# Performance work log

Hardware: AMD Instinct MI355X
Metric: run time of the kernel (lower is better)

Reference implementation:

```python
import jax, jax.numpy as jnp
import numpy as np

B, T, C, H = 16, 2048, 768, 128

def setup_inputs() -> dict:
    key = jax.random.key(0)
    k1, k2, k3, k4 = jax.random.split(key, 4)
    x = jax.random.normal(k1, (B, T, C), dtype=jnp.float32)
    Wq = jax.random.normal(k2, (C, H), dtype=jnp.float32) * (C ** -0.5)
    Wk = jax.random.normal(k3, (C, H), dtype=jnp.float32) * (C ** -0.5)
    Wv = jax.random.normal(k4, (C, H), dtype=jnp.float32) * (C ** -0.5)
    return {"x": x, "Wq": Wq, "Wk": Wk, "Wv": Wv}

def reference(x, Wq, Wk, Wv):
    Bc, Tc, Cc = x.shape
    q = jnp.einsum('btc,ch->bth', x, Wq)
    k = jnp.einsum('btc,ch->bth', x, Wk)
    v = jnp.einsum('btc,ch->bth', x, Wv)
    wei = jnp.einsum('bqh,bkh->bqk', q, k)  # [B,T,T]
    tril = jnp.tril(jnp.ones((Tc, Tc), dtype=jnp.float32))
    # Faithful to original: mask with -inf FIRST, then scale by C**-0.5
    wei = jnp.where(tril == 0, -jnp.inf, wei) * (Cc ** -0.5)
    wei = jax.nn.softmax(wei, axis=-1)
    out = jnp.einsum('bqk,bkh->bqh', wei, v)
    return out
```

## Files before the change

kernel.cpp:

```cpp
#include <hip/hip_runtime.h>
#include <hip/hip_bf16.h>
#include <cstdint>

#define B_ 16
#define T_ 2048
#define C_ 768
#define H_ 128

typedef __bf16 bf16x8 __attribute__((ext_vector_type(8)));
typedef float f32x4 __attribute__((ext_vector_type(4)));
typedef unsigned short u16x8 __attribute__((ext_vector_type(8)));

__device__ __forceinline__ void gld_lds16(const void* g, void* s) {
    __builtin_amdgcn_global_load_lds(
        (__attribute__((address_space(1))) void*)(size_t)g,
        (__attribute__((address_space(3))) void*)s,
        16, 0, 0);
}

__device__ __forceinline__ unsigned short f2bf(float f) {
    __bf16 h = (__bf16)f;
    return __builtin_bit_cast(unsigned short, h);
}

__global__ __launch_bounds__(256) void wconv_kernel(
    const float* __restrict__ Wq, const float* __restrict__ Wk,
    const float* __restrict__ Wv, unsigned short* __restrict__ wT) {
    int idx = blockIdx.x * 256 + threadIdx.x;
    if (idx >= 3 * H_ * C_) return;
    int w = idx / (H_ * C_);
    int r = idx % (H_ * C_);
    int h = r / C_;
    int c = r % C_;
    const float* W = (w == 0) ? Wq : ((w == 1) ? Wk : Wv);
    wT[idx] = f2bf(W[c * H_ + h]);
}

__global__ __launch_bounds__(512, 2) void proj_kernel(
    const float* __restrict__ x, const unsigned short* __restrict__ wT,
    unsigned short* __restrict__ qb, unsigned short* __restrict__ kb,
    unsigned short* __restrict__ vtb) {
    __shared__ unsigned short Asm[2][128 * 64];
    __shared__ unsigned short Bsm[2][192 * 64];

    const int tid = threadIdx.x;
    const int nh = blockIdx.x & 1;
    const int m0 = (blockIdx.x >> 1) * 128;
    const int wid = tid >> 6;
    const int lane = tid & 63;
    const int quad = lane >> 4;
    const int lo16 = lane & 15;
    const int mh = (wid >> 2) * 64;
    const int wnl = (wid & 3) * 48;
    const unsigned short* wTn = wT + (size_t)nh * 192 * C_;

    const int am0 = (tid * 2) >> 4;
    (void)am0;

    f32x4 acc[4][3] = {};
    f32x4 pre[4];

#pragma unroll
    for (int r = 0; r < 2; ++r) {
        int cidx = r * 512 + tid;
        int m = cidx >> 3, lc = cidx & 7;
        const float* src = x + (size_t)(m0 + m) * C_ + lc * 8;
        pre[r * 2] = *(const f32x4*)src;
        pre[r * 2 + 1] = *(const f32x4*)(src + 4);
    }
#pragma unroll
    for (int r = 0; r < 3; ++r) {
        int cidx = r * 512 + tid;
        int n = cidx >> 3, c = (cidx & 7) ^ (n & 7);
        gld_lds16((const char*)wTn + ((size_t)n * C_ + c * 8) * 2,
                  (char*)&Bsm[0][0] + (r * 512 + wid * 64) * 16);
    }
#pragma unroll
    for (int r = 0; r < 2; ++r) {
        int cidx = r * 512 + tid;
        int m = cidx >> 3, lc = cidx & 7;
        u16x8 o;
        o[0] = f2bf(pre[r * 2][0]); o[1] = f2bf(pre[r * 2][1]);
        o[2] = f2bf(pre[r * 2][2]); o[3] = f2bf(pre[r * 2][3]);
        o[4] = f2bf(pre[r * 2 + 1][0]); o[5] = f2bf(pre[r * 2 + 1][1]);
        o[6] = f2bf(pre[r * 2 + 1][2]); o[7] = f2bf(pre[r * 2 + 1][3]);
        *(u16x8*)(&Asm[0][m * 64 + (lc ^ (m & 7)) * 8]) = o;
    }

    for (int kt = 0; kt < 12; ++kt) {
        const int p = kt & 1;
        __syncthreads();
        if (kt + 1 < 12) {
            const int k1 = (kt + 1) * 64;
#pragma unroll
            for (int r = 0; r < 2; ++r) {
                int cidx = r * 512 + tid;
                int m = cidx >> 3, lc = cidx & 7;
                const float* src = x + (size_t)(m0 + m) * C_ + k1 + lc * 8;
                pre[r * 2] = *(const f32x4*)src;
                pre[r * 2 + 1] = *(const f32x4*)(src + 4);
            }
#pragma unroll
            for (int r = 0; r < 3; ++r) {
                int cidx = r * 512 + tid;
                int n = cidx >> 3, c = (cidx & 7) ^ (n & 7);
                gld_lds16((const char*)wTn + ((size_t)n * C_ + k1 + c * 8) * 2,
                          (char*)&Bsm[p ^ 1][0] + (r * 512 + wid * 64) * 16);
            }
        }

#pragma unroll
        for (int kk = 0; kk < 2; ++kk) {
            bf16x8 af[4], bf[3];
#pragma unroll
            for (int mi = 0; mi < 4; ++mi) {
                int m = mh + mi * 16 + lo16;
                int c = (kk * 4 + quad) ^ (m & 7);
                af[mi] = *(const bf16x8*)((const __bf16*)&Asm[p][0] + m * 64 + c * 8);
            }
#pragma unroll
            for (int ni = 0; ni < 3; ++ni) {
                int n = wnl + ni * 16 + lo16;
                int c = (kk * 4 + quad) ^ (n & 7);
                bf[ni] = *(const bf16x8*)((const __bf16*)&Bsm[p][0] + n * 64 + c * 8);
            }
#pragma unroll
            for (int mi = 0; mi < 4; ++mi)
#pragma unroll
                for (int ni = 0; ni < 3; ++ni)
                    acc[mi][ni] = __builtin_amdgcn_mfma_f32_16x16x32_bf16(
                        af[mi], bf[ni], acc[mi][ni], 0, 0, 0);
        }

        if (kt + 1 < 12) {
#pragma unroll
            for (int r = 0; r < 2; ++r) {
                int cidx = r * 512 + tid;
                int m = cidx >> 3, lc = cidx & 7;
                u16x8 o;
                o[0] = f2bf(pre[r * 2][0]); o[1] = f2bf(pre[r * 2][1]);
                o[2] = f2bf(pre[r * 2][2]); o[3] = f2bf(pre[r * 2][3]);
                o[4] = f2bf(pre[r * 2 + 1][0]); o[5] = f2bf(pre[r * 2 + 1][1]);
                o[6] = f2bf(pre[r * 2 + 1][2]); o[7] = f2bf(pre[r * 2 + 1][3]);
                *(u16x8*)(&Asm[p ^ 1][m * 64 + (lc ^ (m & 7)) * 8]) = o;
            }
        }
    }

#pragma unroll
    for (int mi = 0; mi < 4; ++mi) {
        int grow = m0 + mh + mi * 16 + quad * 4;
#pragma unroll
        for (int ni = 0; ni < 3; ++ni) {
            int n = nh * 192 + wnl + ni * 16 + lo16;
            int wmat = n >> 7;
            int col = n & 127;
            if (wmat < 2) {
                unsigned short* o = (wmat == 0) ? qb : kb;
#pragma unroll
                for (int rr = 0; rr < 4; ++rr)
                    o[(size_t)(grow + rr) * H_ + col] = f2bf(acc[mi][ni][rr]);
            } else {
                int b = grow >> 11;
                int t = grow & 2047;
                ushort4 pk;
                pk.x = f2bf(acc[mi][ni][0]); pk.y = f2bf(acc[mi][ni][1]);
                pk.z = f2bf(acc[mi][ni][2]); pk.w = f2bf(acc[mi][ni][3]);
                *(ushort4*)(vtb + ((size_t)b * H_ + col) * T_ + t) = pk;
            }
        }
    }
}

__device__ __forceinline__ void attn_stage(
    const unsigned short* kB, const unsigned short* vB, int kv0, int p,
    unsigned short* Ks, unsigned short* Vs, int tid, int wid) {
#pragma unroll
    for (int rnd = 0; rnd < 4; ++rnd) {
        int cidx = rnd * 256 + tid;
        int m = cidx >> 4;
        int c = (cidx & 15) ^ (m & 15);
        gld_lds16((const char*)kB + ((size_t)(kv0 + m) * H_ + c * 8) * 2,
                  (char*)(Ks + p * 64 * 128) + (rnd * 256 + wid * 64) * 16);
    }
#pragma unroll
    for (int rnd = 0; rnd < 4; ++rnd) {
        int cidx = rnd * 256 + tid;
        int d = cidx >> 3;
        int c = (cidx & 7) ^ (d & 7);
        gld_lds16((const char*)vB + ((size_t)d * T_ + kv0 + c * 8) * 2,
                  (char*)(Vs + p * 128 * 64) + (rnd * 256 + wid * 64) * 16);
    }
}

__device__ __forceinline__ void attn_seg(
    const unsigned short* kB, const unsigned short* vB, const bf16x8 qfrag[4],
    int j0, int j1, int jmask, float& l_part, f32x4 oacc[8],
    unsigned short* Ks, unsigned short* Vs, unsigned short* Pw,
    int tid, int wid, int quad, int lo16) {
    const float cs = 0.05205877694341f;
    __syncthreads();
    attn_stage(kB, vB, j0 * 64, 0, Ks, Vs, tid, wid);
    for (int j = j0; j < j1; ++j) {
        const int p = (j - j0) & 1;
        __syncthreads();
        if (j + 1 < j1) attn_stage(kB, vB, (j + 1) * 64, p ^ 1, Ks, Vs, tid, wid);

        const unsigned short* Kp = Ks + p * 64 * 128;
        const unsigned short* Vp = Vs + p * 128 * 64;

        f32x4 s[4] = {};
#pragma unroll
        for (int ks = 0; ks < 4; ++ks) {
#pragma unroll
            for (int ni = 0; ni < 4; ++ni) {
                int row = ni * 16 + lo16;
                int slot = (ks * 4 + quad) ^ lo16;
                bf16x8 kf = *(const bf16x8*)((const __bf16*)Kp + row * 128 + slot * 8);
                s[ni] = __builtin_amdgcn_mfma_f32_16x16x32_bf16(kf, qfrag[ks], s[ni], 0, 0, 0);
            }
        }

        const bool diag = (j == jmask);
        if (diag) {
#pragma unroll
            for (int ni = 0; ni < 4; ++ni) {
#pragma unroll
                for (int rr = 0; rr < 4; ++rr) {
                    float pv = exp2f(s[ni][rr] * cs);
                    if (ni * 16 + quad * 4 + rr > wid * 16 + lo16) pv = 0.f;
                    l_part += pv;
                    s[ni][rr] = pv;
                }
                ushort4 w4;
                w4.x = f2bf(s[ni][0]); w4.y = f2bf(s[ni][1]);
                w4.z = f2bf(s[ni][2]); w4.w = f2bf(s[ni][3]);
                *(ushort4*)(Pw + lo16 * 72 + ni * 16 + quad * 4) = w4;
            }
        } else {
#pragma unroll
            for (int ni = 0; ni < 4; ++ni) {
#pragma unroll
                for (int rr = 0; rr < 4; ++rr) {
                    float pv = exp2f(s[ni][rr] * cs);
                    l_part += pv;
                    s[ni][rr] = pv;
                }
                ushort4 w4;
                w4.x = f2bf(s[ni][0]); w4.y = f2bf(s[ni][1]);
                w4.z = f2bf(s[ni][2]); w4.w = f2bf(s[ni][3]);
                *(ushort4*)(Pw + lo16 * 72 + ni * 16 + quad * 4) = w4;
            }
        }

#pragma unroll
        for (int ks2 = 0; ks2 < 2; ++ks2) {
            bf16x8 pf = *(const bf16x8*)((const __bf16*)Pw + lo16 * 72 + ks2 * 32 + quad * 8);
#pragma unroll
            for (int nd = 0; nd < 8; ++nd) {
                int dn = nd * 16 + lo16;
                int vc = (ks2 * 4 + quad) ^ (dn & 7);
                bf16x8 vf = *(const bf16x8*)((const __bf16*)Vp + dn * 64 + vc * 8);
                oacc[nd] = __builtin_amdgcn_mfma_f32_16x16x32_bf16(pf, vf, oacc[nd], 0, 0, 0);
            }
        }
    }
}

__device__ __forceinline__ void load_qfrag(const unsigned short* qB, int q0,
                                           int wid, int quad, int lo16, bf16x8 qf[4]) {
    const unsigned short* qrow = qB + (size_t)(q0 + wid * 16 + lo16) * H_ + quad * 8;
#pragma unroll
    for (int ks = 0; ks < 4; ++ks) qf[ks] = *(const bf16x8*)(qrow + ks * 32);
}

__global__ __launch_bounds__(256, 2) void attn_kernel(
    const unsigned short* __restrict__ qb, const unsigned short* __restrict__ kb,
    const unsigned short* __restrict__ vtb, float* __restrict__ out,
    float* __restrict__ pO, float* __restrict__ pL) {
    __shared__ unsigned short Ks[2][64 * 128];
    __shared__ unsigned short Vs[2][128 * 64];
    __shared__ unsigned short Ps[4][16 * 72];

    const int tid = threadIdx.x;
    const int bid = blockIdx.x;
    const int half = bid >> 8;
    const int slot = bid & 255;
    const int r = slot >> 4;
    const int b = slot & 15;

    const unsigned short* qB = qb + (size_t)b * T_ * H_;
    const unsigned short* kB = kb + (size_t)b * T_ * H_;
    const unsigned short* vB = vtb + (size_t)b * H_ * T_;

    const int wid = tid >> 6;
    const int lane = tid & 63;
    const int quad = lane >> 4;
    const int lo16 = lane & 15;
    unsigned short* Pw = &Ps[wid][0];

    const int qtb = 31 - r;
    bf16x8 qf[4];
    float l_part = 0.f;
    f32x4 oacc[8] = {};

    if (half == 0) {
        load_qfrag(qB, r * 64, wid, quad, lo16, qf);
        attn_seg(kB, vB, qf, 0, r + 1, r, l_part, oacc, &Ks[0][0], &Vs[0][0], Pw,
                 tid, wid, quad, lo16);
        l_part += __shfl_xor(l_part, 16);
        l_part += __shfl_xor(l_part, 32);
#pragma unroll
        for (int rr = 0; rr < 4; ++rr) {
            float lv = __shfl(l_part, quad * 4 + rr);
            float inv = 1.0f / lv;
            int qrow = r * 64 + wid * 16 + quad * 4 + rr;
            float* orow = out + ((size_t)b * T_ + qrow) * H_;
#pragma unroll
            for (int nd = 0; nd < 8; ++nd)
                orow[nd * 16 + lo16] = oacc[nd][rr] * inv;
        }
        l_part = 0.f;
#pragma unroll
        for (int nd = 0; nd < 8; ++nd) oacc[nd] = f32x4{0.f, 0.f, 0.f, 0.f};
        load_qfrag(qB, qtb * 64, wid, quad, lo16, qf);
        attn_seg(kB, vB, qf, 0, 16 - r, -1, l_part, oacc, &Ks[0][0], &Vs[0][0], Pw,
                 tid, wid, quad, lo16);
    } else {
        load_qfrag(qB, qtb * 64, wid, quad, lo16, qf);
        attn_seg(kB, vB, qf, 16 - r, 32 - r, qtb, l_part, oacc, &Ks[0][0], &Vs[0][0], Pw,
                 tid, wid, quad, lo16);
    }

    l_part += __shfl_xor(l_part, 16);
    l_part += __shfl_xor(l_part, 32);
    float* myO = pO + (size_t)(half * 256 + slot) * (64 * 128);
    if (lane < 16) pL[(half * 256 + slot) * 64 + wid * 16 + lo16] = l_part;
#pragma unroll
    for (int rr = 0; rr < 4; ++rr) {
        int ql = wid * 16 + quad * 4 + rr;
#pragma unroll
        for (int nd = 0; nd < 8; ++nd)
            myO[ql * 128 + nd * 16 + lo16] = oacc[nd][rr];
    }
}

__global__ __launch_bounds__(256) void combine_kernel(
    const float* __restrict__ pO, const float* __restrict__ pL,
    float* __restrict__ out) {
    const int slot = blockIdx.x;
    const int r = slot >> 4;
    const int b = slot & 15;
    const int q0 = (31 - r) * 64;
    __shared__ float ls[64];
    const int tid = threadIdx.x;
    if (tid < 64) ls[tid] = pL[slot * 64 + tid] + pL[(256 + slot) * 64 + tid];
    __syncthreads();
    const float* O0 = pO + (size_t)slot * (64 * 128);
    const float* O1 = pO + (size_t)(256 + slot) * (64 * 128);
    float* ob = out + ((size_t)b * T_ + q0) * H_;
#pragma unroll
    for (int k = 0; k < 8; ++k) {
        int idx = (k * 256 + tid) * 4;
        f32x4 a = *(const f32x4*)(O0 + idx);
        f32x4 c = *(const f32x4*)(O1 + idx);
        float inv = 1.0f / ls[idx >> 7];
        f32x4 o;
        o[0] = (a[0] + c[0]) * inv; o[1] = (a[1] + c[1]) * inv;
        o[2] = (a[2] + c[2]) * inv; o[3] = (a[3] + c[3]) * inv;
        *(f32x4*)(ob + idx) = o;
    }
}

extern "C" void kernel_launch(void* const* d_in, const int* in_sizes, int n_in,
                              void* d_out, int out_size, void* d_ws, size_t ws_size,
                              hipStream_t stream) {
    const float* x = (const float*)d_in[0];
    const float* Wq = (const float*)d_in[1];
    const float* Wk = (const float*)d_in[2];
    const float* Wv = (const float*)d_in[3];
    float* out = (float*)d_out;

    char* ws = (char*)d_ws;
    unsigned short* wT  = (unsigned short*)ws;
    unsigned short* qb  = (unsigned short*)(ws + (1ull << 20));
    unsigned short* kb  = (unsigned short*)(ws + (9ull << 20));
    unsigned short* vtb = (unsigned short*)(ws + (17ull << 20));
    float* pO = (float*)(ws + (80ull << 20));
    float* pL = (float*)(ws + (100ull << 20));

    hipLaunchKernelGGL(wconv_kernel, dim3(1152), dim3(256), 0, stream, Wq, Wk, Wv, wT);
    hipLaunchKernelGGL(proj_kernel, dim3(512), dim3(512), 0, stream, x, wT, qb, kb, vtb);
    hipLaunchKernelGGL(attn_kernel, dim3(512), dim3(256), 0, stream, qb, kb, vtb, out, pO, pL);
    hipLaunchKernelGGL(combine_kernel, dim3(256), dim3(256), 0, stream, pO, pL, out);
}
```

Baseline: 208.7 us.

## Split attention KV tile across two wave groups with LDS cross-group reduction

The attention block grows from 4 to 8 waves. Each pair of waves shares a 16-row query group, and each wave in the pair handles half of the 64-key tile (32 keys). The partial O accumulators and row sums are then reduced through LDS, reusing the K buffer, before the output is written. This doubles the waves available to hide latency and halves the serial MFMA chain per wave, at the cost of extra LDS traffic and syncs for the reduction and higher block-level register/LDS pressure.

```diff
diff --git a/kernel.cpp b/kernel.cpp
--- a/kernel.cpp
+++ b/kernel.cpp
@@ -54,9 +54,6 @@
     const int wnl = (wid & 3) * 48;
     const unsigned short* wTn = wT + (size_t)nh * 192 * C_;
 
-    const int am0 = (tid * 2) >> 4;
-    (void)am0;
-
     f32x4 acc[4][3] = {};
     f32x4 pre[4];
 
@@ -176,20 +173,20 @@
     const unsigned short* kB, const unsigned short* vB, int kv0, int p,
     unsigned short* Ks, unsigned short* Vs, int tid, int wid) {
 #pragma unroll
-    for (int rnd = 0; rnd < 4; ++rnd) {
-        int cidx = rnd * 256 + tid;
+    for (int rnd = 0; rnd < 2; ++rnd) {
+        int cidx = rnd * 512 + tid;
         int m = cidx >> 4;
         int c = (cidx & 15) ^ (m & 15);
         gld_lds16((const char*)kB + ((size_t)(kv0 + m) * H_ + c * 8) * 2,
-                  (char*)(Ks + p * 64 * 128) + (rnd * 256 + wid * 64) * 16);
-    }
-#pragma unroll
-    for (int rnd = 0; rnd < 4; ++rnd) {
-        int cidx = rnd * 256 + tid;
+                  (char*)(Ks + p * 64 * 128) + (rnd * 512 + wid * 64) * 16);
+    }
+#pragma unroll
+    for (int rnd = 0; rnd < 2; ++rnd) {
+        int cidx = rnd * 512 + tid;
         int d = cidx >> 3;
         int c = (cidx & 7) ^ (d & 7);
         gld_lds16((const char*)vB + ((size_t)d * T_ + kv0 + c * 8) * 2,
-                  (char*)(Vs + p * 128 * 64) + (rnd * 256 + wid * 64) * 16);
+                  (char*)(Vs + p * 128 * 64) + (rnd * 512 + wid * 64) * 16);
     }
 }
 
@@ -197,7 +194,7 @@
     const unsigned short* kB, const unsigned short* vB, const bf16x8 qfrag[4],
     int j0, int j1, int jmask, float& l_part, f32x4 oacc[8],
     unsigned short* Ks, unsigned short* Vs, unsigned short* Pw,
-    int tid, int wid, int quad, int lo16) {
+    int tid, int wid, int quad, int lo16, int qg, int kvh) {
     const float cs = 0.05205877694341f;
     __syncthreads();
     attn_stage(kB, vB, j0 * 64, 0, Ks, Vs, tid, wid);
@@ -209,12 +206,12 @@
         const unsigned short* Kp = Ks + p * 64 * 128;
         const unsigned short* Vp = Vs + p * 128 * 64;
 
-        f32x4 s[4] = {};
+        f32x4 s[2] = {};
 #pragma unroll
         for (int ks = 0; ks < 4; ++ks) {
 #pragma unroll
-            for (int ni = 0; ni < 4; ++ni) {
-                int row = ni * 16 + lo16;
+            for (int ni = 0; ni < 2; ++ni) {
+                int row = kvh * 32 + ni * 16 + lo16;
                 int slot = (ks * 4 + quad) ^ lo16;
                 bf16x8 kf = *(const bf16x8*)((const __bf16*)Kp + row * 128 + slot * 8);
                 s[ni] = __builtin_amdgcn_mfma_f32_16x16x32_bf16(kf, qfrag[ks], s[ni], 0, 0, 0);
@@ -224,22 +221,22 @@
         const bool diag = (j == jmask);
         if (diag) {
 #pragma unroll
-            for (int ni = 0; ni < 4; ++ni) {
+            for (int ni = 0; ni < 2; ++ni) {
 #pragma unroll
                 for (int rr = 0; rr < 4; ++rr) {
                     float pv = exp2f(s[ni][rr] * cs);
-                    if (ni * 16 + quad * 4 + rr > wid * 16 + lo16) pv = 0.f;
+                    if (kvh * 32 + ni * 16 + quad * 4 + rr > qg * 16 + lo16) pv = 0.f;
                     l_part += pv;
                     s[ni][rr] = pv;
                 }
                 ushort4 w4;
                 w4.x = f2bf(s[ni][0]); w4.y = f2bf(s[ni][1]);
                 w4.z = f2bf(s[ni][2]); w4.w = f2bf(s[ni][3]);
-                *(ushort4*)(Pw + lo16 * 72 + ni * 16 + quad * 4) = w4;
+                *(ushort4*)(Pw + lo16 * 40 + ni * 16 + quad * 4) = w4;
             }
         } else {
 #pragma unroll
-            for (int ni = 0; ni < 4; ++ni) {
+            for (int ni = 0; ni < 2; ++ni) {
 #pragma unroll
                 for (int rr = 0; rr < 4; ++rr) {
                     float pv = exp2f(s[ni][rr] * cs);
@@ -249,38 +246,63 @@
                 ushort4 w4;
                 w4.x = f2bf(s[ni][0]); w4.y = f2bf(s[ni][1]);
                 w4.z = f2bf(s[ni][2]); w4.w = f2bf(s[ni][3]);
-                *(ushort4*)(Pw + lo16 * 72 + ni * 16 + quad * 4) = w4;
-            }
-        }
-
-#pragma unroll
-        for (int ks2 = 0; ks2 < 2; ++ks2) {
-            bf16x8 pf = *(const bf16x8*)((const __bf16*)Pw + lo16 * 72 + ks2 * 32 + quad * 8);
-#pragma unroll
-            for (int nd = 0; nd < 8; ++nd) {
-                int dn = nd * 16 + lo16;
-                int vc = (ks2 * 4 + quad) ^ (dn & 7);
-                bf16x8 vf = *(const bf16x8*)((const __bf16*)Vp + dn * 64 + vc * 8);
-                oacc[nd] = __builtin_amdgcn_mfma_f32_16x16x32_bf16(pf, vf, oacc[nd], 0, 0, 0);
-            }
+                *(ushort4*)(Pw + lo16 * 40 + ni * 16 + quad * 4) = w4;
+            }
+        }
+
+        bf16x8 pf = *(const bf16x8*)((const __bf16*)Pw + lo16 * 40 + quad * 8);
+#pragma unroll
+        for (int nd = 0; nd < 8; ++nd) {
+            int dn = nd * 16 + lo16;
+            int vc = (kvh * 4 + quad) ^ (dn & 7);
+            bf16x8 vf = *(const bf16x8*)((const __bf16*)Vp + dn * 64 + vc * 8);
+            oacc[nd] = __builtin_amdgcn_mfma_f32_16x16x32_bf16(pf, vf, oacc[nd], 0, 0, 0);
         }
     }
 }
 
 __device__ __forceinline__ void load_qfrag(const unsigned short* qB, int q0,
-                                           int wid, int quad, int lo16, bf16x8 qf[4]) {
-    const unsigned short* qrow = qB + (size_t)(q0 + wid * 16 + lo16) * H_ + quad * 8;
+                                           int qg, int quad, int lo16, bf16x8 qf[4]) {
+    const unsigned short* qrow = qB + (size_t)(q0 + qg * 16 + lo16) * H_ + quad * 8;
 #pragma unroll
     for (int ks = 0; ks < 4; ++ks) qf[ks] = *(const bf16x8*)(qrow + ks * 32);
 }
 
-__global__ __launch_bounds__(256, 2) void attn_kernel(
+__device__ __forceinline__ void xgroup_reduce(
+    float& l_part, f32x4 oacc[8], unsigned short* KsBase, float* Lred,
+    int lane, int qg, int kvh) {
+    l_part += __shfl_xor(l_part, 16);
+    l_part += __shfl_xor(l_part, 32);
+    __syncthreads();
+    float* red = (float*)KsBase;
+    if (kvh == 1) {
+        float* dst = red + (size_t)(qg * 64 + lane) * 32;
+#pragma unroll
+        for (int nd = 0; nd < 8; ++nd)
+            *(f32x4*)(dst + ((nd ^ (lane & 7)) * 4)) = oacc[nd];
+        Lred[qg * 64 + lane] = l_part;
+    }
+    __syncthreads();
+    if (kvh == 0) {
+        const float* src = red + (size_t)(qg * 64 + lane) * 32;
+#pragma unroll
+        for (int nd = 0; nd < 8; ++nd) {
+            f32x4 t = *(const f32x4*)(src + ((nd ^ (lane & 7)) * 4));
+            oacc[nd][0] += t[0]; oacc[nd][1] += t[1];
+            oacc[nd][2] += t[2]; oacc[nd][3] += t[3];
+        }
+        l_part += Lred[qg * 64 + lane];
+    }
+}
+
+__global__ __launch_bounds__(512, 4) void attn_kernel(
     const unsigned short* __restrict__ qb, const unsigned short* __restrict__ kb,
     const unsigned short* __restrict__ vtb, float* __restrict__ out,
     float* __restrict__ pO, float* __restrict__ pL) {
     __shared__ unsigned short Ks[2][64 * 128];
     __shared__ unsigned short Vs[2][128 * 64];
-    __shared__ unsigned short Ps[4][16 * 72];
+    __shared__ unsigned short Ps[8][16 * 40];
+    __shared__ float Lred[256];
 
     const int tid = threadIdx.x;
     const int bid = blockIdx.x;
@@ -297,6 +319,8 @@
     const int lane = tid & 63;
     const int quad = lane >> 4;
     const int lo16 = lane & 15;
+    const int qg = wid & 3;
+    const int kvh = wid >> 2;
     unsigned short* Pw = &Ps[wid][0];
 
     const int qtb = 31 - r;
@@ -305,43 +329,45 @@
     f32x4 oacc[8] = {};
 
     if (half == 0) {
-        load_qfrag(qB, r * 64, wid, quad, lo16, qf);
+        load_qfrag(qB, r * 64, qg, quad, lo16, qf);
         attn_seg(kB, vB, qf, 0, r + 1, r, l_part, oacc, &Ks[0][0], &Vs[0][0], Pw,
-                 tid, wid, quad, lo16);
-        l_part += __shfl_xor(l_part, 16);
-        l_part += __shfl_xor(l_part, 32);
+                 tid, wid, quad, lo16, qg, kvh);
+        xgroup_reduce(l_part, oacc, &Ks[0][0], Lred, lane, qg, kvh);
+        if (kvh == 0) {
+#pragma unroll
+            for (int rr = 0; rr < 4; ++rr) {
+                float lv = __shfl(l_part, quad * 4 + rr);
+                float inv = 1.0f / lv;
+                int qrow = r * 64 + qg * 16 + quad * 4 + rr;
+                float* orow = out + ((size_t)b * T_ + qrow) * H_;
+#pragma unroll
+                for (int nd = 0; nd < 8; ++nd)
+                    orow[nd * 16 + lo16] = oacc[nd][rr] * inv;
+            }
+        }
+        l_part = 0.f;
+#pragma unroll
+        for (int nd = 0; nd < 8; ++nd) oacc[nd] = f32x4{0.f, 0.f, 0.f, 0.f};
+        load_qfrag(qB, qtb * 64, qg, quad, lo16, qf);
+        attn_seg(kB, vB, qf, 0, 16 - r, -1, l_part, oacc, &Ks[0][0], &Vs[0][0], Pw,
+                 tid, wid, quad, lo16, qg, kvh);
+    } else {
+        load_qfrag(qB, qtb * 64, qg, quad, lo16, qf);
+        attn_seg(kB, vB, qf, 16 - r, 32 - r, qtb, l_part, oacc, &Ks[0][0], &Vs[0][0], Pw,
+                 tid, wid, quad, lo16, qg, kvh);
+    }
+
+    xgroup_reduce(l_part, oacc, &Ks[0][0], Lred, lane, qg, kvh);
+    if (kvh == 0) {
+        float* myO = pO + (size_t)(half * 256 + slot) * (64 * 128);
+        if (lane < 16) pL[(half * 256 + slot) * 64 + qg * 16 + lo16] = l_part;
 #pragma unroll
         for (int rr = 0; rr < 4; ++rr) {
-            float lv = __shfl(l_part, quad * 4 + rr);
-            float inv = 1.0f / lv;
-            int qrow = r * 64 + wid * 16 + quad * 4 + rr;
-            float* orow = out + ((size_t)b * T_ + qrow) * H_;
+            int ql = qg * 16 + quad * 4 + rr;
 #pragma unroll
             for (int nd = 0; nd < 8; ++nd)
-                orow[nd * 16 + lo16] = oacc[nd][rr] * inv;
-        }
-        l_part = 0.f;
-#pragma unroll
-        for (int nd = 0; nd < 8; ++nd) oacc[nd] = f32x4{0.f, 0.f, 0.f, 0.f};
-        load_qfrag(qB, qtb * 64, wid, quad, lo16, qf);
-        attn_seg(kB, vB, qf, 0, 16 - r, -1, l_part, oacc, &Ks[0][0], &Vs[0][0], Pw,
-                 tid, wid, quad, lo16);
-    } else {
-        load_qfrag(qB, qtb * 64, wid, quad, lo16, qf);
-        attn_seg(kB, vB, qf, 16 - r, 32 - r, qtb, l_part, oacc, &Ks[0][0], &Vs[0][0], Pw,
-                 tid, wid, quad, lo16);
-    }
-
-    l_part += __shfl_xor(l_part, 16);
-    l_part += __shfl_xor(l_part, 32);
-    float* myO = pO + (size_t)(half * 256 + slot) * (64 * 128);
-    if (lane < 16) pL[(half * 256 + slot) * 64 + wid * 16 + lo16] = l_part;
-#pragma unroll
-    for (int rr = 0; rr < 4; ++rr) {
-        int ql = wid * 16 + quad * 4 + rr;
-#pragma unroll
-        for (int nd = 0; nd < 8; ++nd)
-            myO[ql * 128 + nd * 16 + lo16] = oacc[nd][rr];
+                myO[ql * 128 + nd * 16 + lo16] = oacc[nd][rr];
+        }
     }
 }
 
@@ -391,6 +417,6 @@
 
     hipLaunchKernelGGL(wconv_kernel, dim3(1152), dim3(256), 0, stream, Wq, Wk, Wv, wT);
     hipLaunchKernelGGL(proj_kernel, dim3(512), dim3(512), 0, stream, x, wT, qb, kb, vtb);
-    hipLaunchKernelGGL(attn_kernel, dim3(512), dim3(256), 0, stream, qb, kb, vtb, out, pO, pL);
+    hipLaunchKernelGGL(attn_kernel, dim3(512), dim3(512), 0, stream, qb, kb, vtb, out, pO, pL);
     hipLaunchKernelGGL(combine_kernel, dim3(256), dim3(256), 0, stream, pO, pL, out);
 }
```

New measurement: 210.7 us. No clear change (+0.9%).

## Switch attention to 32x32 MFMA with in-register P and split-KV wave reduction

Applied to the files above, without the earlier changes.

Rewrites the attention inner loop to use 32x32x16 bf16 MFMA tiles. The four waves are split into 2 query halves by 2 KV halves, and the two KV halves' partial outputs and row sums are reduced through LDS at the end. The P matrix is packed to bf16 with v_cvt_pk_bf16_f32 and rearranged with v_permlane32_swap, so it stays in registers instead of round-tripping through LDS. The aim is fewer LDS operations and better MFMA efficiency, at the cost of an extra cross-wave reduction with two barriers and higher accumulator register pressure.

```diff
diff --git a/kernel.cpp b/kernel.cpp
--- a/kernel.cpp
+++ b/kernel.cpp
@@ -9,7 +9,9 @@
 
 typedef __bf16 bf16x8 __attribute__((ext_vector_type(8)));
 typedef float f32x4 __attribute__((ext_vector_type(4)));
+typedef float f32x16 __attribute__((ext_vector_type(16)));
 typedef unsigned short u16x8 __attribute__((ext_vector_type(8)));
+typedef unsigned int u32x4 __attribute__((ext_vector_type(4)));
 
 __device__ __forceinline__ void gld_lds16(const void* g, void* s) {
     __builtin_amdgcn_global_load_lds(
@@ -54,9 +56,6 @@
     const int wnl = (wid & 3) * 48;
     const unsigned short* wTn = wT + (size_t)nh * 192 * C_;
 
-    const int am0 = (tid * 2) >> 4;
-    (void)am0;
-
     f32x4 acc[4][3] = {};
     f32x4 pre[4];
 
@@ -194,11 +193,16 @@
 }
 
 __device__ __forceinline__ void attn_seg(
-    const unsigned short* kB, const unsigned short* vB, const bf16x8 qfrag[4],
-    int j0, int j1, int jmask, float& l_part, f32x4 oacc[8],
-    unsigned short* Ks, unsigned short* Vs, unsigned short* Pw,
-    int tid, int wid, int quad, int lo16) {
+    const unsigned short* kB, const unsigned short* vB, const bf16x8 qfrag[8],
+    int j0, int j1, int jmask, int qbase, float& l_part, f32x16 oacc[4],
+    unsigned short* Ks, unsigned short* Vs,
+    int tid, int wid, int lane, int qh, int kvh) {
     const float cs = 0.05205877694341f;
+    const int l31 = lane & 31;
+    const int h8 = lane >> 5;
+    const int rowbase = kvh * 32 + 4 * h8;
+    const int qglob = qbase + l31;
+
     __syncthreads();
     attn_stage(kB, vB, j0 * 64, 0, Ks, Vs, tid, wid);
     for (int j = j0; j < j1; ++j) {
@@ -209,69 +213,106 @@
         const unsigned short* Kp = Ks + p * 64 * 128;
         const unsigned short* Vp = Vs + p * 128 * 64;
 
-        f32x4 s[4] = {};
-#pragma unroll
-        for (int ks = 0; ks < 4; ++ks) {
-#pragma unroll
-            for (int ni = 0; ni < 4; ++ni) {
-                int row = ni * 16 + lo16;
-                int slot = (ks * 4 + quad) ^ lo16;
-                bf16x8 kf = *(const bf16x8*)((const __bf16*)Kp + row * 128 + slot * 8);
-                s[ni] = __builtin_amdgcn_mfma_f32_16x16x32_bf16(kf, qfrag[ks], s[ni], 0, 0, 0);
-            }
-        }
-
-        const bool diag = (j == jmask);
-        if (diag) {
-#pragma unroll
-            for (int ni = 0; ni < 4; ++ni) {
-#pragma unroll
-                for (int rr = 0; rr < 4; ++rr) {
-                    float pv = exp2f(s[ni][rr] * cs);
-                    if (ni * 16 + quad * 4 + rr > wid * 16 + lo16) pv = 0.f;
-                    l_part += pv;
-                    s[ni][rr] = pv;
-                }
-                ushort4 w4;
-                w4.x = f2bf(s[ni][0]); w4.y = f2bf(s[ni][1]);
-                w4.z = f2bf(s[ni][2]); w4.w = f2bf(s[ni][3]);
-                *(ushort4*)(Pw + lo16 * 72 + ni * 16 + quad * 4) = w4;
+        f32x16 s = {};
+        const unsigned short* Kr = Kp + (kvh * 32 + l31) * 128;
+#pragma unroll
+        for (int ks = 0; ks < 8; ++ks) {
+            int g = (ks * 2 + h8) ^ (l31 & 15);
+            bf16x8 kf = *(const bf16x8*)((const __bf16*)Kr + g * 8);
+            s = __builtin_amdgcn_mfma_f32_32x32x16_bf16(kf, qfrag[ks], s, 0, 0, 0);
+        }
+
+        if (j == jmask) {
+#pragma unroll
+            for (int r = 0; r < 16; ++r) {
+                float pv = exp2f(s[r] * cs);
+                int kvg = j * 64 + rowbase + (r & 3) + 8 * (r >> 2);
+                if (kvg > qglob) pv = 0.f;
+                l_part += pv;
+                s[r] = pv;
             }
         } else {
 #pragma unroll
-            for (int ni = 0; ni < 4; ++ni) {
-#pragma unroll
-                for (int rr = 0; rr < 4; ++rr) {
-                    float pv = exp2f(s[ni][rr] * cs);
-                    l_part += pv;
-                    s[ni][rr] = pv;
-                }
-                ushort4 w4;
-                w4.x = f2bf(s[ni][0]); w4.y = f2bf(s[ni][1]);
-                w4.z = f2bf(s[ni][2]); w4.w = f2bf(s[ni][3]);
-                *(ushort4*)(Pw + lo16 * 72 + ni * 16 + quad * 4) = w4;
-            }
-        }
+            for (int r = 0; r < 16; ++r) {
+                float pv = exp2f(s[r] * cs);
+                l_part += pv;
+                s[r] = pv;
+            }
+        }
+
+        unsigned int w0, w1, w2, w3, w4, w5, w6, w7;
+        asm("v_cvt_pk_bf16_f32 %0, %1, %2" : "=v"(w0) : "v"(s[0]), "v"(s[1]));
+        asm("v_cvt_pk_bf16_f32 %0, %1, %2" : "=v"(w1) : "v"(s[2]), "v"(s[3]));
+        asm("v_cvt_pk_bf16_f32 %0, %1, %2" : "=v"(w2) : "v"(s[4]), "v"(s[5]));
+        asm("v_cvt_pk_bf16_f32 %0, %1, %2" : "=v"(w3) : "v"(s[6]), "v"(s[7]));
+        asm("v_cvt_pk_bf16_f32 %0, %1, %2" : "=v"(w4) : "v"(s[8]), "v"(s[9]));
+        asm("v_cvt_pk_bf16_f32 %0, %1, %2" : "=v"(w5) : "v"(s[10]), "v"(s[11]));
+        asm("v_cvt_pk_bf16_f32 %0, %1, %2" : "=v"(w6) : "v"(s[12]), "v"(s[13]));
+        asm("v_cvt_pk_bf16_f32 %0, %1, %2" : "=v"(w7) : "v"(s[14]), "v"(s[15]));
+        asm("v_permlane32_swap_b32 %0, %1" : "+v"(w0), "+v"(w2));
+        asm("v_permlane32_swap_b32 %0, %1" : "+v"(w1), "+v"(w3));
+        asm("v_permlane32_swap_b32 %0, %1" : "+v"(w4), "+v"(w6));
+        asm("v_permlane32_swap_b32 %0, %1" : "+v"(w5), "+v"(w7));
+        u32x4 a0v = {w0, w1, w2, w3};
+        u32x4 a1v = {w4, w5, w6, w7};
+        bf16x8 pa0 = __builtin_bit_cast(bf16x8, a0v);
+        bf16x8 pa1 = __builtin_bit_cast(bf16x8, a1v);
 
 #pragma unroll
         for (int ks2 = 0; ks2 < 2; ++ks2) {
-            bf16x8 pf = *(const bf16x8*)((const __bf16*)Pw + lo16 * 72 + ks2 * 32 + quad * 8);
-#pragma unroll
-            for (int nd = 0; nd < 8; ++nd) {
-                int dn = nd * 16 + lo16;
-                int vc = (ks2 * 4 + quad) ^ (dn & 7);
-                bf16x8 vf = *(const bf16x8*)((const __bf16*)Vp + dn * 64 + vc * 8);
-                oacc[nd] = __builtin_amdgcn_mfma_f32_16x16x32_bf16(pf, vf, oacc[nd], 0, 0, 0);
+            bf16x8 pf = (ks2 == 0) ? pa0 : pa1;
+#pragma unroll
+            for (int dblk = 0; dblk < 4; ++dblk) {
+                int d = dblk * 32 + l31;
+                int vg = (kvh * 4 + ks2 * 2 + h8) ^ (d & 7);
+                bf16x8 vf = *(const bf16x8*)((const __bf16*)Vp + d * 64 + vg * 8);
+                oacc[dblk] = __builtin_amdgcn_mfma_f32_32x32x16_bf16(pf, vf, oacc[dblk], 0, 0, 0);
             }
         }
     }
 }
 
 __device__ __forceinline__ void load_qfrag(const unsigned short* qB, int q0,
-                                           int wid, int quad, int lo16, bf16x8 qf[4]) {
-    const unsigned short* qrow = qB + (size_t)(q0 + wid * 16 + lo16) * H_ + quad * 8;
-#pragma unroll
-    for (int ks = 0; ks < 4; ++ks) qf[ks] = *(const bf16x8*)(qrow + ks * 32);
+                                           int qh, int lane, bf16x8 qf[8]) {
+    const int l31 = lane & 31, h8 = lane >> 5;
+    const unsigned short* qrow = qB + (size_t)(q0 + qh * 32 + l31) * H_ + h8 * 8;
+#pragma unroll
+    for (int ks = 0; ks < 8; ++ks) qf[ks] = *(const bf16x8*)(qrow + ks * 16);
+}
+
+__device__ __forceinline__ void xgroup_reduce(
+    float& l_part, f32x16 oacc[4], unsigned short* KsBase, float* Lred,
+    int lane, int qh, int kvh) {
+    l_part += __shfl_xor(l_part, 32);
+    __syncthreads();
+    float* base = (float*)KsBase + (size_t)(qh * 64 + lane) * 64;
+    if (kvh == 1) {
+#pragma unroll
+        for (int dblk = 0; dblk < 4; ++dblk)
+#pragma unroll
+            for (int part = 0; part < 4; ++part) {
+                int c = dblk * 4 + part;
+                f32x4 v = {oacc[dblk][part * 4 + 0], oacc[dblk][part * 4 + 1],
+                           oacc[dblk][part * 4 + 2], oacc[dblk][part * 4 + 3]};
+                *(f32x4*)(base + ((c ^ (lane & 15)) * 4)) = v;
+            }
+        if (lane < 32) Lred[qh * 32 + lane] = l_part;
+    }
+    __syncthreads();
+    if (kvh == 0) {
+#pragma unroll
+        for (int dblk = 0; dblk < 4; ++dblk)
+#pragma unroll
+            for (int part = 0; part < 4; ++part) {
+                int c = dblk * 4 + part;
+                f32x4 v = *(const f32x4*)(base + ((c ^ (lane & 15)) * 4));
+                oacc[dblk][part * 4 + 0] += v[0];
+                oacc[dblk][part * 4 + 1] += v[1];
+                oacc[dblk][part * 4 + 2] += v[2];
+                oacc[dblk][part * 4 + 3] += v[3];
+            }
+        l_part += Lred[qh * 32 + (lane & 31)];
+    }
 }
 
 __global__ __launch_bounds__(256, 2) void attn_kernel(
@@ -280,7 +321,7 @@
     float* __restrict__ pO, float* __restrict__ pL) {
     __shared__ unsigned short Ks[2][64 * 128];
     __shared__ unsigned short Vs[2][128 * 64];
-    __shared__ unsigned short Ps[4][16 * 72];
+    __shared__ float Lred[64];
 
     const int tid = threadIdx.x;
     const int bid = blockIdx.x;
@@ -295,53 +336,58 @@
 
     const int wid = tid >> 6;
     const int lane = tid & 63;
-    const int quad = lane >> 4;
-    const int lo16 = lane & 15;
-    unsigned short* Pw = &Ps[wid][0];
+    const int l31 = lane & 31;
+    const int h8 = lane >> 5;
+    const int qh = wid & 1;
+    const int kvh = wid >> 1;
 
     const int qtb = 31 - r;
-    bf16x8 qf[4];
+    bf16x8 qf[8];
     float l_part = 0.f;
-    f32x4 oacc[8] = {};
+    f32x16 oacc[4] = {};
 
     if (half == 0) {
-        load_qfrag(qB, r * 64, wid, quad, lo16, qf);
-        attn_seg(kB, vB, qf, 0, r + 1, r, l_part, oacc, &Ks[0][0], &Vs[0][0], Pw,
-                 tid, wid, quad, lo16);
-        l_part += __shfl_xor(l_part, 16);
-        l_part += __shfl_xor(l_part, 32);
-#pragma unroll
-        for (int rr = 0; rr < 4; ++rr) {
-            float lv = __shfl(l_part, quad * 4 + rr);
-            float inv = 1.0f / lv;
-            int qrow = r * 64 + wid * 16 + quad * 4 + rr;
-            float* orow = out + ((size_t)b * T_ + qrow) * H_;
-#pragma unroll
-            for (int nd = 0; nd < 8; ++nd)
-                orow[nd * 16 + lo16] = oacc[nd][rr] * inv;
+        load_qfrag(qB, r * 64, qh, lane, qf);
+        attn_seg(kB, vB, qf, 0, r + 1, r, r * 64 + qh * 32, l_part, oacc,
+                 &Ks[0][0], &Vs[0][0], tid, wid, lane, qh, kvh);
+        xgroup_reduce(l_part, oacc, &Ks[0][0], Lred, lane, qh, kvh);
+        if (kvh == 0) {
+            float* outb = out + (size_t)b * T_ * H_;
+#pragma unroll
+            for (int rr = 0; rr < 16; ++rr) {
+                int ql = (rr & 3) + 8 * (rr >> 2) + 4 * h8;
+                float inv = 1.0f / __shfl(l_part, ql);
+                float* orow = outb + (size_t)(r * 64 + qh * 32 + ql) * H_;
+#pragma unroll
+                for (int dblk = 0; dblk < 4; ++dblk)
+                    orow[dblk * 32 + l31] = oacc[dblk][rr] * inv;
+            }
         }
         l_part = 0.f;
 #pragma unroll
-        for (int nd = 0; nd < 8; ++nd) oacc[nd] = f32x4{0.f, 0.f, 0.f, 0.f};
-        load_qfrag(qB, qtb * 64, wid, quad, lo16, qf);
-        attn_seg(kB, vB, qf, 0, 16 - r, -1, l_part, oacc, &Ks[0][0], &Vs[0][0], Pw,
-                 tid, wid, quad, lo16);
+        for (int dblk = 0; dblk < 4; ++dblk)
+#pragma unroll
+            for (int e = 0; e < 16; ++e) oacc[dblk][e] = 0.f;
+        load_qfrag(qB, qtb * 64, qh, lane, qf);
+        attn_seg(kB, vB, qf, 0, 16 - r, -1, qtb * 64 + qh * 32, l_part, oacc,
+                 &Ks[0][0], &Vs[0][0], tid, wid, lane, qh, kvh);
     } else {
-        load_qfrag(qB, qtb * 64, wid, quad, lo16, qf);
-        attn_seg(kB, vB, qf, 16 - r, 32 - r, qtb, l_part, oacc, &Ks[0][0], &Vs[0][0], Pw,
-                 tid, wid, quad, lo16);
-    }
-
-    l_part += __shfl_xor(l_part, 16);
-    l_part += __shfl_xor(l_part, 32);
-    float* myO = pO + (size_t)(half * 256 + slot) * (64 * 128);
-    if (lane < 16) pL[(half * 256 + slot) * 64 + wid * 16 + lo16] = l_part;
-#pragma unroll
-    for (int rr = 0; rr < 4; ++rr) {
-        int ql = wid * 16 + quad * 4 + rr;
-#pragma unroll
-        for (int nd = 0; nd < 8; ++nd)
-            myO[ql * 128 + nd * 16 + lo16] = oacc[nd][rr];
+        load_qfrag(qB, qtb * 64, qh, lane, qf);
+        attn_seg(kB, vB, qf, 16 - r, 32 - r, qtb, qtb * 64 + qh * 32, l_part, oacc,
+                 &Ks[0][0], &Vs[0][0], tid, wid, lane, qh, kvh);
+    }
+
+    xgroup_reduce(l_part, oacc, &Ks[0][0], Lred, lane, qh, kvh);
+    if (kvh == 0) {
+        float* myO = pO + (size_t)(half * 256 + slot) * (64 * 128);
+        if (lane < 32) pL[(half * 256 + slot) * 64 + qh * 32 + lane] = l_part;
+#pragma unroll
+        for (int rr = 0; rr < 16; ++rr) {
+            int ql = qh * 32 + (rr & 3) + 8 * (rr >> 2) + 4 * h8;
+#pragma unroll
+            for (int dblk = 0; dblk < 4; ++dblk)
+                myO[ql * 128 + dblk * 32 + l31] = oacc[dblk][rr];
+        }
     }
 }
 
```

Measured after the change: 209.1 us. No clear change (+0.2%).
